# Performance work log

Measured on AMD Instinct MI355X. Metric: run time of the kernel, lower is better.

Reference implementation:

```python
import jax, jax.numpy as jnp
import numpy as np
import math

D = 1024  # output_dim (power of 2)
IN = 1024  # input dim
CAP = int(math.log2(D))  # number of butterfly stages


def _gen_indices(s):
    """Static FFT-butterfly index lists (numpy, computed at trace time)."""
    def ind_s(k):
        if k == 0:
            return [np.array([1, 0])]
        temp = np.arange(2 ** k)
        list0 = [np.concatenate([temp + 2 ** k, temp])]
        list1 = ind_s(k - 1)
        for i in range(k):
            list0.append(np.concatenate([list1[i], list1[i] + 2 ** k]))
        return list0

    t = ind_s(int(math.log2(s // 2)))
    cap = int(math.log2(s))
    ind_exe = [np.asarray(t[i], dtype=np.int32) for i in range(cap)]
    ind_param = []
    for i in range(cap):
        ind = np.concatenate([np.arange(0, s, 2 ** i) + j for j in range(2 ** i)]).astype(np.int32)
        ind_param.append(ind)
    return ind_exe, ind_param


IND_EXE, IND_PARAM = _gen_indices(D)


def setup_inputs() -> dict:
    key = jax.random.key(0)
    ks = jax.random.split(key, 9)
    B = 8192
    x = jax.random.normal(ks[0], (B, IN), dtype=jnp.float32)
    state = jax.random.normal(ks[1], (B, D), dtype=jnp.float32)
    theta = jax.random.uniform(ks[2], (CAP, D // 2), minval=-3.14, maxval=3.14, dtype=jnp.float32)
    U = jax.random.uniform(ks[3], (IN, 3 * D), minval=-0.01, maxval=0.01, dtype=jnp.float32)
    W_r = jax.random.uniform(ks[4], (D, D), minval=-0.01, maxval=0.01, dtype=jnp.float32)
    W_g = jax.random.uniform(ks[5], (D, D), minval=-0.01, maxval=0.01, dtype=jnp.float32)
    bias_r = jnp.full((D,), 2.0, dtype=jnp.float32)
    bias_g = jnp.zeros((D,), dtype=jnp.float32)
    bias_c = jnp.full((D,), 0.01, dtype=jnp.float32)
    return {"x": x, "state": state, "theta": theta, "U": U, "W_r": W_r,
            "W_g": W_g, "bias_r": bias_r, "bias_g": bias_g, "bias_c": bias_c}


def reference(x, state, theta, U, W_r, W_g, bias_r, bias_g, bias_c):
    # fft_param: rotation coefficients, permuted by the static ind_param lists
    cos_list = jnp.concatenate([jnp.cos(theta), jnp.cos(theta)], axis=1)   # [CAP, D]
    sin_list = jnp.concatenate([jnp.sin(theta), -jnp.sin(theta)], axis=1)  # [CAP, D]
    v1 = jnp.stack([cos_list[i][IND_PARAM[i]] for i in range(CAP)])  # [CAP, D]
    v2 = jnp.stack([sin_list[i][IND_PARAM[i]] for i in range(CAP)])  # [CAP, D]

    Ux = x @ U                                   # [B, 3D]
    U_cx, U_rx, U_gx = jnp.split(Ux, 3, axis=1)  # each [B, D]
    r = jax.nn.sigmoid(U_rx + state @ W_r + bias_r)
    g = jax.nn.sigmoid(U_gx + state @ W_g + bias_g)

    # butterfly orthogonal rotation of the state
    h = state
    for i in range(CAP):
        h = h * v1[i] + (h * v2[i])[:, IND_EXE[i]]

    # modReLU
    pre = r * h + U_cx
    c = jnp.sign(pre) * jax.nn.relu(jnp.abs(pre) + 0.001 + bias_c)

    out = g * state + (1.0 - g) * c
    return out
```

## Files before the change

### kernel.cpp

```cpp
#include <hip/hip_runtime.h>
#include <hip/hip_bf16.h>
#include <stdint.h>


typedef __bf16 bf16x8 __attribute__((ext_vector_type(8)));
typedef __bf16 bf16x4 __attribute__((ext_vector_type(4)));
typedef __bf16 bf16x2 __attribute__((ext_vector_type(2)));
typedef float f32x4 __attribute__((ext_vector_type(4)));

#define B_ROWS 8192

__device__ __forceinline__ void async16(__bf16* lds, const __hip_bfloat16* g) {
    __builtin_amdgcn_global_load_lds((const __attribute__((address_space(1))) void*)g,
                                     (__attribute__((address_space(3))) void*)lds,
                                     16, 0, 0);
}

__global__ __launch_bounds__(256) void prep_all(const float* __restrict__ x,
                                                const float* __restrict__ state,
                                                const float* __restrict__ theta,
                                                const float* __restrict__ U,
                                                const float* __restrict__ Wr,
                                                const float* __restrict__ Wg,
                                                __hip_bfloat16* __restrict__ xs,
                                                __hip_bfloat16* __restrict__ Wt0,
                                                __hip_bfloat16* __restrict__ Wt12,
                                                float* __restrict__ v1,
                                                float* __restrict__ v2) {
    __shared__ float tile[32][33];
    const int id = blockIdx.x;
    if (id < 8192) {
        const int row = id;
        const int col = threadIdx.x * 8;
        const float* src = (col < 1024) ? (x + (size_t)row * 1024 + col)
                                        : (state + (size_t)row * 1024 + (col - 1024));
        float4 a = *(const float4*)src;
        float4 b = *(const float4*)(src + 4);
        bf16x8 v;
        v[0] = (__bf16)a.x; v[1] = (__bf16)a.y; v[2] = (__bf16)a.z; v[3] = (__bf16)a.w;
        v[4] = (__bf16)b.x; v[5] = (__bf16)b.y; v[6] = (__bf16)b.z; v[7] = (__bf16)b.w;
        *(bf16x8*)((__bf16*)xs + (size_t)row * 2048 + col) = v;
    } else if (id < 13312) {
        const int wid = id - 8192;
        const float* src; int srcN, scol, sk;
        __hip_bfloat16* dst; int dstStride, dn, dk;
        bool ilv;
        if (wid < 1024) {
            int nx = wid & 31, ky = wid >> 5;
            src = U; srcN = 3072; scol = nx * 32; sk = ky * 32;
            dst = Wt0; dstStride = 1024; dn = nx * 32; dk = ky * 32;
            ilv = false;
        } else {
            int id2 = wid - 1024;
            int nx = id2 & 63, ky = id2 >> 6;
            int n0 = nx * 32, k0 = ky * 32;
            dst = Wt12; dstStride = 2048; dn = n0; dk = k0;
            ilv = true;
            if (k0 < 1024)      { src = U;  srcN = 3072; scol = 1024 + n0; sk = k0; }
            else if (n0 < 1024) { src = Wr; srcN = 1024; scol = n0;        sk = k0 - 1024; }
            else                { src = Wg; srcN = 1024; scol = n0 - 1024; sk = k0 - 1024; }
        }
        const int tx = threadIdx.x & 31, ty = threadIdx.x >> 5;
#pragma unroll
        for (int s = 0; s < 4; ++s)
            tile[ty + s * 8][tx] = src[(size_t)(sk + ty + s * 8) * srcN + scol + tx];
        __syncthreads();
#pragma unroll
        for (int s = 0; s < 4; ++s) {
            int n = dn + ty + s * 8;
            int wrow = ilv ? ((n < 1024) ? 2 * n : 2 * (n - 1024) + 1) : n;
            dst[(size_t)wrow * dstStride + dk + tx] = __float2bfloat16(tile[tx][ty + s * 8]);
        }
    } else {
        int idx = (id - 13312) * 256 + threadIdx.x;
        int i = idx >> 10;
        int j = idx & 1023;
        int Q = 1024 >> i;
        int j0 = j / Q;
        int m = j & (Q - 1);
        int q = (m << i) + j0;
        float th = theta[i * 512 + (q & 511)];
        float c = cosf(th);
        float s = sinf(th);
        v1[idx] = c;
        v2[idx] = (q < 512) ? s : -s;
    }
}

#define BAR()   asm volatile("s_barrier" ::: "memory")
#define LGKM0() asm volatile("s_waitcnt lgkmcnt(0)" ::: "memory")
#define LGKM8() asm volatile("s_waitcnt lgkmcnt(8)" ::: "memory")
#define VMCNT(n) asm volatile("s_waitcnt vmcnt(" #n ")" ::: "memory")

__global__ __launch_bounds__(512, 2) void gemm_fused(const __hip_bfloat16* __restrict__ xs,
                                                     const __hip_bfloat16* __restrict__ Wt0,
                                                     const __hip_bfloat16* __restrict__ Wt12,
                                                     const float* __restrict__ bias_r,
                                                     const float* __restrict__ bias_g,
                                                     __hip_bfloat16* __restrict__ P) {
    __shared__ __align__(16) __bf16 As[2][16384];
    __shared__ __align__(16) __bf16 Bs[2][16384];

    const int bid = blockIdx.x;
    const int swz = (bid & 7) * 32 + (bid >> 3);
    const int nt = swz & 7;
    const int mt = swz >> 3;
    const int mBase = mt * 256;

    const int t = threadIdx.x;
    const int lane = t & 63;
    const int wv = t >> 6;
    const int wm = wv & 1;
    const int wn = wv >> 1;
    const int r0 = lane & 15;
    const int gq = lane >> 4;

    const int coff0 = ((gq ^ (r0 & 7)) << 3);
    const int coff1 = coff0 ^ 32;
    const int rowA = wm * 128 + r0;
    const int rowB = wn * 64 + r0;
    const int rowBu = wn * 32 + r0;

    const int s_row = t >> 3;
    const int s_q8 = (((t & 7) ^ (s_row & 7)) << 3);

    const __hip_bfloat16* Ag = xs + (size_t)(mBase + s_row) * 2048 + s_q8;
    const __hip_bfloat16* Bg = Wt12 + (size_t)(nt * 256 + s_row) * 2048 + s_q8;
    const __hip_bfloat16* Cg = Wt0 + (size_t)(nt * 128 + s_row) * 1024 + s_q8;

#define STG_A(buf, h, kt) do { \
    async16(&As[buf][(((h) << 10) + t) << 3],       Ag + (size_t)((h) * 128) * 2048 + (kt) * 64); \
    async16(&As[buf][(((h) << 10) + 512 + t) << 3], Ag + (size_t)((h) * 128 + 64) * 2048 + (kt) * 64); \
} while (0)
#define STG_B(buf, h, kt) do { \
    async16(&Bs[buf][(((h) << 10) + t) << 3],       Bg + (size_t)((h) * 128) * 2048 + (kt) * 64); \
    async16(&Bs[buf][(((h) << 10) + 512 + t) << 3], Bg + (size_t)((h) * 128 + 64) * 2048 + (kt) * 64); \
} while (0)
#define STG_C(buf, kt) do { \
    async16(&Bs[buf][t << 3],         Cg + (kt) * 64); \
    async16(&Bs[buf][(512 + t) << 3], Cg + (size_t)64 * 1024 + (kt) * 64); \
} while (0)

#define LOAD_AFL(bufArr) do { _Pragma("unroll") for (int i = 0; i < 4; ++i) { \
    afl[i][0] = *(const bf16x8*)&bufArr[(rowA + i * 16) * 64 + coff0]; \
    afl[i][1] = *(const bf16x8*)&bufArr[(rowA + i * 16) * 64 + coff1]; } } while (0)
#define LOAD_AFH(bufArr) do { _Pragma("unroll") for (int i = 0; i < 4; ++i) { \
    afh[i][0] = *(const bf16x8*)&bufArr[(rowA + 64 + i * 16) * 64 + coff0]; \
    afh[i][1] = *(const bf16x8*)&bufArr[(rowA + 64 + i * 16) * 64 + coff1]; } } while (0)
#define LOAD_BB(bufArr, base) do { _Pragma("unroll") for (int j = 0; j < 2; ++j) { \
    bb[j][0] = *(const bf16x8*)&bufArr[((base) + j * 16) * 64 + coff0]; \
    bb[j][1] = *(const bf16x8*)&bufArr[((base) + j * 16) * 64 + coff1]; } } while (0)
#define MFMA8(I0, J0, af) do { _Pragma("unroll") for (int i = 0; i < 4; ++i) \
    _Pragma("unroll") for (int j = 0; j < 2; ++j) { \
    acc[(I0) + i][(J0) + j] = __builtin_amdgcn_mfma_f32_16x16x32_bf16(af[i][0], bb[j][0], acc[(I0) + i][(J0) + j], 0, 0, 0); \
    acc[(I0) + i][(J0) + j] = __builtin_amdgcn_mfma_f32_16x16x32_bf16(af[i][1], bb[j][1], acc[(I0) + i][(J0) + j], 0, 0, 0); } } while (0)

    f32x4 acc[8][4];
    bf16x8 afl[4][2], afh[4][2], bb[2][2];
    const f32x4 zero = {0.f, 0.f, 0.f, 0.f};
#pragma unroll
    for (int i = 0; i < 8; ++i)
#pragma unroll
        for (int j = 0; j < 4; ++j) acc[i][j] = zero;

    STG_A(0, 0, 0); STG_A(0, 1, 0);
    STG_B(0, 0, 0); STG_B(0, 1, 0);
    STG_A(1, 0, 1); STG_A(1, 1, 1);
    VMCNT(4);
    BAR();

#pragma unroll 1
    for (int u = 0; u < 16; ++u) {
        const int kt1 = 2 * u + 1;
        const int kt2 = (2 * u + 2) & 31;
        const int kt3 = (2 * u + 3) & 31;

        LOAD_AFL(As[0]);
        LOAD_BB(Bs[0], rowB);
        STG_B(1, 0, kt1);
        LGKM8();
        BAR(); LGKM0();
        __builtin_amdgcn_s_setprio(1); MFMA8(0, 0, afl); __builtin_amdgcn_s_setprio(0);
        BAR();
        LOAD_AFH(As[0]);
        STG_B(1, 1, kt1);
        BAR(); LGKM0();
        __builtin_amdgcn_s_setprio(1); MFMA8(4, 0, afh); __builtin_amdgcn_s_setprio(0);
        BAR();
        LOAD_BB(Bs[0], rowB + 32);
        STG_A(0, 0, kt2);
        BAR(); LGKM0();
        __builtin_amdgcn_s_setprio(1); MFMA8(0, 2, afl); __builtin_amdgcn_s_setprio(0);
        BAR();
        STG_A(0, 1, kt2);
        BAR();
        __builtin_amdgcn_s_setprio(1); MFMA8(4, 2, afh); __builtin_amdgcn_s_setprio(0);
        VMCNT(4);
        BAR();
        LOAD_AFL(As[1]);
        LOAD_BB(Bs[1], rowB);
        STG_B(0, 0, kt2);
        LGKM8();
        BAR(); LGKM0();
        __builtin_amdgcn_s_setprio(1); MFMA8(0, 0, afl); __builtin_amdgcn_s_setprio(0);
        BAR();
        LOAD_AFH(As[1]);
        STG_B(0, 1, kt2);
        BAR(); LGKM0();
        __builtin_amdgcn_s_setprio(1); MFMA8(4, 0, afh); __builtin_amdgcn_s_setprio(0);
        BAR();
        LOAD_BB(Bs[1], rowB + 32);
        STG_A(1, 0, kt3);
        BAR(); LGKM0();
        __builtin_amdgcn_s_setprio(1); MFMA8(0, 2, afl); __builtin_amdgcn_s_setprio(0);
        BAR();
        STG_A(1, 1, kt3);
        BAR();
        __builtin_amdgcn_s_setprio(1); MFMA8(4, 2, afh); __builtin_amdgcn_s_setprio(0);
        VMCNT(4);
        BAR();
    }

    VMCNT(0);
    BAR();

    STG_A(0, 0, 0); STG_A(0, 1, 0);
    STG_C(0, 0);
    STG_C(1, 1);

#pragma unroll
    for (int j = 0; j < 4; ++j) {
        const int ct = nt * 256 + wn * 64 + j * 16 + r0;
        const float bias = (r0 & 1) ? bias_g[ct >> 1] : bias_r[ct >> 1];
#pragma unroll
        for (int i = 0; i < 8; ++i) {
#pragma unroll
            for (int reg = 0; reg < 4; ++reg) {
                const int row = mBase + wm * 128 + i * 16 + gq * 4 + reg;
                const float z = 1.0f / (1.0f + __expf(-(acc[i][j][reg] + bias)));
                P[(size_t)row * 3072 + 1024 + ct] = __float2bfloat16(z);
            }
        }
    }

    VMCNT(0);
    BAR();

#pragma unroll
    for (int i = 0; i < 8; ++i)
#pragma unroll
        for (int j = 0; j < 2; ++j) acc[i][j] = zero;

#pragma unroll 1
    for (int u = 0; u < 8; ++u) {
        const int kt1 = 2 * u + 1;
        const int kt2 = (2 * u + 2) & 15;
        const int kt3 = (2 * u + 3) & 15;

        LOAD_AFL(As[0]);
        LOAD_BB(Bs[0], rowBu);
        STG_A(1, 0, kt1); STG_A(1, 1, kt1);
        LGKM8();
        BAR(); LGKM0();
        __builtin_amdgcn_s_setprio(1); MFMA8(0, 0, afl); __builtin_amdgcn_s_setprio(0);
        BAR();
        LOAD_AFH(As[0]);
        STG_C(0, kt2);
        BAR(); LGKM0();
        __builtin_amdgcn_s_setprio(1); MFMA8(4, 0, afh); __builtin_amdgcn_s_setprio(0);
        VMCNT(2);
        BAR();
        LOAD_AFL(As[1]);
        LOAD_BB(Bs[1], rowBu);
        STG_A(0, 0, kt2); STG_A(0, 1, kt2);
        LGKM8();
        BAR(); LGKM0();
        __builtin_amdgcn_s_setprio(1); MFMA8(0, 0, afl); __builtin_amdgcn_s_setprio(0);
        BAR();
        LOAD_AFH(As[1]);
        STG_C(1, kt3);
        BAR(); LGKM0();
        __builtin_amdgcn_s_setprio(1); MFMA8(4, 0, afh); __builtin_amdgcn_s_setprio(0);
        VMCNT(2);
        BAR();
    }

#pragma unroll
    for (int j = 0; j < 2; ++j) {
        const int col = nt * 128 + wn * 32 + j * 16 + r0;
#pragma unroll
        for (int i = 0; i < 8; ++i) {
#pragma unroll
            for (int reg = 0; reg < 4; ++reg) {
                const int row = mBase + wm * 128 + i * 16 + gq * 4 + reg;
                P[(size_t)row * 3072 + col] = __float2bfloat16(acc[i][j][reg]);
            }
        }
    }
    VMCNT(0);
}

#undef STG_A
#undef STG_B
#undef STG_C
#undef LOAD_AFL
#undef LOAD_AFH
#undef LOAD_BB
#undef MFMA8

__global__ __launch_bounds__(256) void fuse_kernel(const float* __restrict__ state,
                                                   const __hip_bfloat16* __restrict__ P,
                                                   const float* __restrict__ v1,
                                                   const float* __restrict__ v2,
                                                   const float* __restrict__ bias_c,
                                                   float* __restrict__ out) {
    __shared__ float hbuf[8][1024];
    const int t = threadIdx.x;
    const int rowBase = blockIdx.x * 8;

    float h[8][4];
    float sv[8][4];
#pragma unroll
    for (int r = 0; r < 8; ++r) {
        float4 s4 = ((const float4*)(state + (size_t)(rowBase + r) * 1024))[t];
        h[r][0] = s4.x; h[r][1] = s4.y; h[r][2] = s4.z; h[r][3] = s4.w;
        sv[r][0] = s4.x; sv[r][1] = s4.y; sv[r][2] = s4.z; sv[r][3] = s4.w;
        *(float4*)&hbuf[r][4 * t] = s4;
    }

    {
        __syncthreads();
        float4 w1 = *(const float4*)&v1[4 * t];
        float4 w2 = *(const float4*)&v2[4 * (t ^ 128)];
        const float w1v[4] = {w1.x, w1.y, w1.z, w1.w};
        const float w2v[4] = {w2.x, w2.y, w2.z, w2.w};
#pragma unroll
        for (int r = 0; r < 8; ++r) {
            float4 pr = *(const float4*)&hbuf[r][4 * (t ^ 128)];
            const float pv[4] = {pr.x, pr.y, pr.z, pr.w};
#pragma unroll
            for (int e = 0; e < 4; ++e) h[r][e] = h[r][e] * w1v[e] + pv[e] * w2v[e];
        }
        __syncthreads();
    }
    {
#pragma unroll
        for (int r = 0; r < 8; ++r)
            *(float4*)&hbuf[r][4 * t] = (float4){h[r][0], h[r][1], h[r][2], h[r][3]};
        __syncthreads();
        float4 w1 = *(const float4*)&v1[1024 + 4 * t];
        float4 w2 = *(const float4*)&v2[1024 + 4 * (t ^ 64)];
        const float w1v[4] = {w1.x, w1.y, w1.z, w1.w};
        const float w2v[4] = {w2.x, w2.y, w2.z, w2.w};
#pragma unroll
        for (int r = 0; r < 8; ++r) {
            float4 pr = *(const float4*)&hbuf[r][4 * (t ^ 64)];
            const float pv[4] = {pr.x, pr.y, pr.z, pr.w};
#pragma unroll
            for (int e = 0; e < 4; ++e) h[r][e] = h[r][e] * w1v[e] + pv[e] * w2v[e];
        }
    }
#pragma unroll
    for (int i = 2; i <= 7; ++i) {
        const int H = 512 >> i;
        const int lm = H >> 2;
        float4 w1 = *(const float4*)&v1[i * 1024 + 4 * t];
        float4 w2 = *(const float4*)&v2[i * 1024 + 4 * (t ^ lm)];
        const float w1v[4] = {w1.x, w1.y, w1.z, w1.w};
        const float w2v[4] = {w2.x, w2.y, w2.z, w2.w};
#pragma unroll
        for (int r = 0; r < 8; ++r) {
#pragma unroll
            for (int e = 0; e < 4; ++e) {
                float p = __shfl_xor(h[r][e], lm, 64);
                h[r][e] = h[r][e] * w1v[e] + p * w2v[e];
            }
        }
    }
    {
        float4 w1 = *(const float4*)&v1[8 * 1024 + 4 * t];
        float4 w2 = *(const float4*)&v2[8 * 1024 + 4 * t];
        const float w1v[4] = {w1.x, w1.y, w1.z, w1.w};
        const float w2v[4] = {w2.x, w2.y, w2.z, w2.w};
#pragma unroll
        for (int r = 0; r < 8; ++r) {
            float nh[4];
#pragma unroll
            for (int e = 0; e < 4; ++e) nh[e] = h[r][e] * w1v[e] + h[r][e ^ 2] * w2v[e ^ 2];
#pragma unroll
            for (int e = 0; e < 4; ++e) h[r][e] = nh[e];
        }
        float4 u1 = *(const float4*)&v1[9 * 1024 + 4 * t];
        float4 u2 = *(const float4*)&v2[9 * 1024 + 4 * t];
        const float u1v[4] = {u1.x, u1.y, u1.z, u1.w};
        const float u2v[4] = {u2.x, u2.y, u2.z, u2.w};
#pragma unroll
        for (int r = 0; r < 8; ++r) {
            float nh[4];
#pragma unroll
            for (int e = 0; e < 4; ++e) nh[e] = h[r][e] * u1v[e] + h[r][e ^ 1] * u2v[e ^ 1];
#pragma unroll
            for (int e = 0; e < 4; ++e) h[r][e] = nh[e];
        }
    }

    const float4 bc = ((const float4*)bias_c)[t];
    const float bcv[4] = {bc.x, bc.y, bc.z, bc.w};
#pragma unroll
    for (int r = 0; r < 8; ++r) {
        const int row = rowBase + r;
        const __hip_bfloat16* Pr = P + (size_t)row * 3072;
        bf16x4 ux = *(const bf16x4*)((const __bf16*)Pr + 4 * t);
        bf16x8 rg = *(const bf16x8*)((const __bf16*)Pr + 1024 + 8 * t);
        float o[4];
#pragma unroll
        for (int e = 0; e < 4; ++e) {
            float Ucx = (float)ux[e];
            float rr  = (float)rg[2 * e];
            float gg  = (float)rg[2 * e + 1];
            float pre = rr * h[r][e] + Ucx;
            float mag = fabsf(pre) + 0.001f + bcv[e];
            float c = (pre > 0.f) ? mag : ((pre < 0.f) ? -mag : 0.f);
            o[e] = gg * sv[r][e] + (1.f - gg) * c;
        }
        ((float4*)(out + (size_t)row * 1024))[t] = (float4){o[0], o[1], o[2], o[3]};
    }
}

extern "C" void kernel_launch(void* const* d_in, const int* in_sizes, int n_in,
                              void* d_out, int out_size, void* d_ws, size_t ws_size,
                              hipStream_t stream) {
    const float* x      = (const float*)d_in[0];
    const float* state  = (const float*)d_in[1];
    const float* theta  = (const float*)d_in[2];
    const float* U      = (const float*)d_in[3];
    const float* W_r    = (const float*)d_in[4];
    const float* W_g    = (const float*)d_in[5];
    const float* bias_r = (const float*)d_in[6];
    const float* bias_g = (const float*)d_in[7];
    const float* bias_c = (const float*)d_in[8];
    float* out = (float*)d_out;

    __hip_bfloat16* xs   = (__hip_bfloat16*)d_ws;
    __hip_bfloat16* Wt0  = xs + (size_t)B_ROWS * 2048;
    __hip_bfloat16* Wt12 = Wt0 + (size_t)1024 * 1024;
    __hip_bfloat16* P    = Wt12 + (size_t)2048 * 2048;
    float* v1 = (float*)(P + (size_t)B_ROWS * 3072);
    float* v2 = v1 + 10 * 1024;

    prep_all<<<13352, 256, 0, stream>>>(x, state, theta, U, W_r, W_g, xs, Wt0, Wt12, v1, v2);
    gemm_fused<<<256, 512, 0, stream>>>(xs, Wt0, Wt12, bias_r, bias_g, P);
    fuse_kernel<<<1024, 256, 0, stream>>>(state, P, v1, v2, bias_c, out);
}
```

Baseline: 242.9 us.

## Software-pipeline LDS fragment loads across MFMA phases with double-buffered B fragments

Restructures the main GEMM loop so LDS fragment reads for the next MFMA phase are issued before the current phase's MFMAs, using a second B-fragment register set and partial lgkmcnt waits instead of full drains. Sched barriers pin the ordering so the compiler cannot hoist or merge around the waits. The second GEMM loop issues all A/B fragment loads up front, and the epilogue stores are reordered so each row's columns are written together. This aims to hide LDS latency behind MFMA execution, at the cost of more live registers and tighter wait-count bookkeeping that could break correctness if the counts are wrong.

```diff
diff --git a/kernel.cpp b/kernel.cpp
--- a/kernel.cpp
+++ b/kernel.cpp
@@ -87,10 +87,12 @@
     }
 }
 
-#define BAR()   asm volatile("s_barrier" ::: "memory")
-#define LGKM0() asm volatile("s_waitcnt lgkmcnt(0)" ::: "memory")
-#define LGKM8() asm volatile("s_waitcnt lgkmcnt(8)" ::: "memory")
+#define BAR()    asm volatile("s_barrier" ::: "memory")
+#define LGKM(n)  asm volatile("s_waitcnt lgkmcnt(" #n ")" ::: "memory")
 #define VMCNT(n) asm volatile("s_waitcnt vmcnt(" #n ")" ::: "memory")
+#define SCHEDB() __builtin_amdgcn_sched_barrier(0)
+#define PRIO1()  __builtin_amdgcn_s_setprio(1)
+#define PRIO0()  __builtin_amdgcn_s_setprio(0)
 
 __global__ __launch_bounds__(512, 2) void gemm_fused(const __hip_bfloat16* __restrict__ xs,
                                                      const __hip_bfloat16* __restrict__ Wt0,
@@ -141,22 +143,19 @@
     async16(&Bs[buf][(512 + t) << 3], Cg + (size_t)64 * 1024 + (kt) * 64); \
 } while (0)
 
-#define LOAD_AFL(bufArr) do { _Pragma("unroll") for (int i = 0; i < 4; ++i) { \
-    afl[i][0] = *(const bf16x8*)&bufArr[(rowA + i * 16) * 64 + coff0]; \
-    afl[i][1] = *(const bf16x8*)&bufArr[(rowA + i * 16) * 64 + coff1]; } } while (0)
-#define LOAD_AFH(bufArr) do { _Pragma("unroll") for (int i = 0; i < 4; ++i) { \
-    afh[i][0] = *(const bf16x8*)&bufArr[(rowA + 64 + i * 16) * 64 + coff0]; \
-    afh[i][1] = *(const bf16x8*)&bufArr[(rowA + 64 + i * 16) * 64 + coff1]; } } while (0)
-#define LOAD_BB(bufArr, base) do { _Pragma("unroll") for (int j = 0; j < 2; ++j) { \
-    bb[j][0] = *(const bf16x8*)&bufArr[((base) + j * 16) * 64 + coff0]; \
-    bb[j][1] = *(const bf16x8*)&bufArr[((base) + j * 16) * 64 + coff1]; } } while (0)
-#define MFMA8(I0, J0, af) do { _Pragma("unroll") for (int i = 0; i < 4; ++i) \
-    _Pragma("unroll") for (int j = 0; j < 2; ++j) { \
-    acc[(I0) + i][(J0) + j] = __builtin_amdgcn_mfma_f32_16x16x32_bf16(af[i][0], bb[j][0], acc[(I0) + i][(J0) + j], 0, 0, 0); \
-    acc[(I0) + i][(J0) + j] = __builtin_amdgcn_mfma_f32_16x16x32_bf16(af[i][1], bb[j][1], acc[(I0) + i][(J0) + j], 0, 0, 0); } } while (0)
+#define LOAD_AF(dst, bufArr, rbase) do { _Pragma("unroll") for (int i_ = 0; i_ < 4; ++i_) { \
+    dst[i_][0] = *(const bf16x8*)&bufArr[((rbase) + i_ * 16) * 64 + coff0]; \
+    dst[i_][1] = *(const bf16x8*)&bufArr[((rbase) + i_ * 16) * 64 + coff1]; } } while (0)
+#define LOAD_BF(dst, bufArr, rbase) do { _Pragma("unroll") for (int j_ = 0; j_ < 2; ++j_) { \
+    dst[j_][0] = *(const bf16x8*)&bufArr[((rbase) + j_ * 16) * 64 + coff0]; \
+    dst[j_][1] = *(const bf16x8*)&bufArr[((rbase) + j_ * 16) * 64 + coff1]; } } while (0)
+#define MFMA8(I0, J0, af, bf_) do { _Pragma("unroll") for (int i_ = 0; i_ < 4; ++i_) \
+    _Pragma("unroll") for (int j_ = 0; j_ < 2; ++j_) { \
+    acc[(I0) + i_][(J0) + j_] = __builtin_amdgcn_mfma_f32_16x16x32_bf16(af[i_][0], bf_[j_][0], acc[(I0) + i_][(J0) + j_], 0, 0, 0); \
+    acc[(I0) + i_][(J0) + j_] = __builtin_amdgcn_mfma_f32_16x16x32_bf16(af[i_][1], bf_[j_][1], acc[(I0) + i_][(J0) + j_], 0, 0, 0); } } while (0)
 
     f32x4 acc[8][4];
-    bf16x8 afl[4][2], afh[4][2], bb[2][2];
+    bf16x8 afl[4][2], afh[4][2], bb0[2][2], bb1[2][2];
     const f32x4 zero = {0.f, 0.f, 0.f, 0.f};
 #pragma unroll
     for (int i = 0; i < 8; ++i)
@@ -168,6 +167,8 @@
     STG_A(1, 0, 1); STG_A(1, 1, 1);
     VMCNT(4);
     BAR();
+    LOAD_AF(afl, As[0], rowA);
+    LOAD_BF(bb0, Bs[0], rowB);
 
 #pragma unroll 1
     for (int u = 0; u < 16; ++u) {
@@ -175,49 +176,47 @@
         const int kt2 = (2 * u + 2) & 31;
         const int kt3 = (2 * u + 3) & 31;
 
-        LOAD_AFL(As[0]);
-        LOAD_BB(Bs[0], rowB);
+        LOAD_AF(afh, As[0], rowA + 64);
         STG_B(1, 0, kt1);
-        LGKM8();
-        BAR(); LGKM0();
-        __builtin_amdgcn_s_setprio(1); MFMA8(0, 0, afl); __builtin_amdgcn_s_setprio(0);
-        BAR();
-        LOAD_AFH(As[0]);
+        BAR(); LGKM(8); SCHEDB();
+        PRIO1(); MFMA8(0, 0, afl, bb0); PRIO0();
+        BAR();
+        LOAD_BF(bb1, Bs[0], rowB + 32);
         STG_B(1, 1, kt1);
-        BAR(); LGKM0();
-        __builtin_amdgcn_s_setprio(1); MFMA8(4, 0, afh); __builtin_amdgcn_s_setprio(0);
-        BAR();
-        LOAD_BB(Bs[0], rowB + 32);
+        BAR(); LGKM(4); SCHEDB();
+        PRIO1(); MFMA8(4, 0, afh, bb0); PRIO0();
+        BAR();
         STG_A(0, 0, kt2);
-        BAR(); LGKM0();
-        __builtin_amdgcn_s_setprio(1); MFMA8(0, 2, afl); __builtin_amdgcn_s_setprio(0);
-        BAR();
+        BAR(); LGKM(0); SCHEDB();
+        PRIO1(); MFMA8(0, 2, afl, bb1); PRIO0();
+        VMCNT(2);
+        BAR();
+        LOAD_AF(afl, As[1], rowA);
+        LOAD_BF(bb0, Bs[1], rowB);
         STG_A(0, 1, kt2);
-        BAR();
-        __builtin_amdgcn_s_setprio(1); MFMA8(4, 2, afh); __builtin_amdgcn_s_setprio(0);
-        VMCNT(4);
-        BAR();
-        LOAD_AFL(As[1]);
-        LOAD_BB(Bs[1], rowB);
+        BAR(); LGKM(12); SCHEDB();
+        PRIO1(); MFMA8(4, 2, afh, bb1); PRIO0();
+        BAR();
+        LOAD_AF(afh, As[1], rowA + 64);
         STG_B(0, 0, kt2);
-        LGKM8();
-        BAR(); LGKM0();
-        __builtin_amdgcn_s_setprio(1); MFMA8(0, 0, afl); __builtin_amdgcn_s_setprio(0);
-        BAR();
-        LOAD_AFH(As[1]);
+        BAR(); LGKM(8); SCHEDB();
+        PRIO1(); MFMA8(0, 0, afl, bb0); PRIO0();
+        BAR();
+        LOAD_BF(bb1, Bs[1], rowB + 32);
         STG_B(0, 1, kt2);
-        BAR(); LGKM0();
-        __builtin_amdgcn_s_setprio(1); MFMA8(4, 0, afh); __builtin_amdgcn_s_setprio(0);
-        BAR();
-        LOAD_BB(Bs[1], rowB + 32);
+        BAR(); LGKM(4); SCHEDB();
+        PRIO1(); MFMA8(4, 0, afh, bb0); PRIO0();
+        BAR();
         STG_A(1, 0, kt3);
-        BAR(); LGKM0();
-        __builtin_amdgcn_s_setprio(1); MFMA8(0, 2, afl); __builtin_amdgcn_s_setprio(0);
-        BAR();
+        BAR(); LGKM(0); SCHEDB();
+        PRIO1(); MFMA8(0, 2, afl, bb1); PRIO0();
+        VMCNT(2);
+        BAR();
+        LOAD_AF(afl, As[0], rowA);
+        LOAD_BF(bb0, Bs[0], rowB);
         STG_A(1, 1, kt3);
-        BAR();
-        __builtin_amdgcn_s_setprio(1); MFMA8(4, 2, afh); __builtin_amdgcn_s_setprio(0);
-        VMCNT(4);
+        BAR(); LGKM(12); SCHEDB();
+        PRIO1(); MFMA8(4, 2, afh, bb1); PRIO0();
         BAR();
     }
 
@@ -228,17 +227,24 @@
     STG_C(0, 0);
     STG_C(1, 1);
 
-#pragma unroll
-    for (int j = 0; j < 4; ++j) {
-        const int ct = nt * 256 + wn * 64 + j * 16 + r0;
-        const float bias = (r0 & 1) ? bias_g[ct >> 1] : bias_r[ct >> 1];
+    {
+        float biasv[4];
+#pragma unroll
+        for (int j = 0; j < 4; ++j) {
+            const int ct = nt * 256 + wn * 64 + j * 16 + r0;
+            biasv[j] = (r0 & 1) ? bias_g[ct >> 1] : bias_r[ct >> 1];
+        }
 #pragma unroll
         for (int i = 0; i < 8; ++i) {
 #pragma unroll
             for (int reg = 0; reg < 4; ++reg) {
                 const int row = mBase + wm * 128 + i * 16 + gq * 4 + reg;
-                const float z = 1.0f / (1.0f + __expf(-(acc[i][j][reg] + bias)));
-                P[(size_t)row * 3072 + 1024 + ct] = __float2bfloat16(z);
+                __bf16* Pr = (__bf16*)P + (size_t)row * 3072 + 1024 + nt * 256 + wn * 64 + r0;
+#pragma unroll
+                for (int j = 0; j < 4; ++j) {
+                    const float z = 1.0f / (1.0f + __expf(-(acc[i][j][reg] + biasv[j])));
+                    Pr[j * 16] = (__bf16)z;
+                }
             }
         }
     }
@@ -257,44 +263,41 @@
         const int kt2 = (2 * u + 2) & 15;
         const int kt3 = (2 * u + 3) & 15;
 
-        LOAD_AFL(As[0]);
-        LOAD_BB(Bs[0], rowBu);
+        LOAD_AF(afl, As[0], rowA);
+        LOAD_BF(bb0, Bs[0], rowBu);
+        LOAD_AF(afh, As[0], rowA + 64);
         STG_A(1, 0, kt1); STG_A(1, 1, kt1);
-        LGKM8();
-        BAR(); LGKM0();
-        __builtin_amdgcn_s_setprio(1); MFMA8(0, 0, afl); __builtin_amdgcn_s_setprio(0);
-        BAR();
-        LOAD_AFH(As[0]);
+        BAR(); LGKM(8); SCHEDB();
+        PRIO1(); MFMA8(0, 0, afl, bb0); PRIO0();
+        BAR();
         STG_C(0, kt2);
-        BAR(); LGKM0();
-        __builtin_amdgcn_s_setprio(1); MFMA8(4, 0, afh); __builtin_amdgcn_s_setprio(0);
+        BAR(); LGKM(0); SCHEDB();
+        PRIO1(); MFMA8(4, 0, afh, bb0); PRIO0();
         VMCNT(2);
         BAR();
-        LOAD_AFL(As[1]);
-        LOAD_BB(Bs[1], rowBu);
+        LOAD_AF(afl, As[1], rowA);
+        LOAD_BF(bb0, Bs[1], rowBu);
+        LOAD_AF(afh, As[1], rowA + 64);
         STG_A(0, 0, kt2); STG_A(0, 1, kt2);
-        LGKM8();
-        BAR(); LGKM0();
-        __builtin_amdgcn_s_setprio(1); MFMA8(0, 0, afl); __builtin_amdgcn_s_setprio(0);
-        BAR();
-        LOAD_AFH(As[1]);
+        BAR(); LGKM(8); SCHEDB();
+        PRIO1(); MFMA8(0, 0, afl, bb0); PRIO0();
+        BAR();
         STG_C(1, kt3);
-        BAR(); LGKM0();
-        __builtin_amdgcn_s_setprio(1); MFMA8(4, 0, afh); __builtin_amdgcn_s_setprio(0);
+        BAR(); LGKM(0); SCHEDB();
+        PRIO1(); MFMA8(4, 0, afh, bb0); PRIO0();
         VMCNT(2);
         BAR();
     }
 
 #pragma unroll
-    for (int j = 0; j < 2; ++j) {
-        const int col = nt * 128 + wn * 32 + j * 16 + r0;
-#pragma unroll
-        for (int i = 0; i < 8; ++i) {
-#pragma unroll
-            for (int reg = 0; reg < 4; ++reg) {
-                const int row = mBase + wm * 128 + i * 16 + gq * 4 + reg;
-                P[(size_t)row * 3072 + col] = __float2bfloat16(acc[i][j][reg]);
-            }
+    for (int i = 0; i < 8; ++i) {
+#pragma unroll
+        for (int reg = 0; reg < 4; ++reg) {
+            const int row = mBase + wm * 128 + i * 16 + gq * 4 + reg;
+            __bf16* Pr = (__bf16*)P + (size_t)row * 3072 + nt * 128 + wn * 32 + r0;
+#pragma unroll
+            for (int j = 0; j < 2; ++j)
+                Pr[j * 16] = (__bf16)(float)acc[i][j][reg];
         }
     }
     VMCNT(0);
@@ -303,9 +306,8 @@
 #undef STG_A
 #undef STG_B
 #undef STG_C
-#undef LOAD_AFL
-#undef LOAD_AFH
-#undef LOAD_BB
+#undef LOAD_AF
+#undef LOAD_BF
 #undef MFMA8
 
 __global__ __launch_bounds__(256) void fuse_kernel(const float* __restrict__ state,
```

Measured after the change: 242.8 us. No clear change (-0.0%).
